# Kernel optimization log

Measured on AMD Instinct MI355X. Metric: run time of the kernel, lower is better.

Reference implementation:

```python
import jax, jax.numpy as jnp
import numpy as np

N, E = 50000, 1600000
C_IN, C_H, C_OUT = 36, 64, 64
EPS = 1e-16  # PyG softmax denominator epsilon


def setup_inputs() -> dict:
    key = jax.random.key(0)
    ks = jax.random.split(key, 48)
    inp = {}
    inp["features"] = jax.random.normal(ks[0], (N, C_IN), dtype=jnp.float32)
    inp["edge_attr"] = jax.random.uniform(ks[1], (E, 1), dtype=jnp.float32)
    inp["edge_index"] = jax.random.randint(ks[2], (2, E), 0, N, dtype=jnp.int32)
    dims = [(C_IN, C_H), (C_H, C_H), (C_H, C_H), (C_H, C_OUT)]
    i = 3
    for l, (din, dout) in enumerate(dims, 1):
        s = 1.0 / np.sqrt(din)
        inp[f"Wl{l}"] = jax.random.normal(ks[i], (din, dout), jnp.float32) * s; i += 1
        inp[f"bl{l}"] = jax.random.normal(ks[i], (dout,), jnp.float32) * 0.02; i += 1
        inp[f"Wr{l}"] = jax.random.normal(ks[i], (din, dout), jnp.float32) * s; i += 1
        inp[f"br{l}"] = jax.random.normal(ks[i], (dout,), jnp.float32) * 0.02; i += 1
        inp[f"We{l}"] = jax.random.normal(ks[i], (1, dout), jnp.float32); i += 1
        inp[f"att{l}"] = jax.random.normal(ks[i], (dout,), jnp.float32) * s; i += 1
        inp[f"bo{l}"] = jax.random.normal(ks[i], (dout,), jnp.float32) * 0.02; i += 1
    mlp = [(C_OUT, C_OUT // 2, "m1"), (C_OUT // 2, C_OUT // 4, "m2"), (C_OUT // 4, 1, "m3")]
    for din, dout, tag in mlp:
        s = 1.0 / np.sqrt(din)
        inp[f"W{tag}"] = jax.random.normal(ks[i], (din, dout), jnp.float32) * s; i += 1
        inp[f"b{tag}"] = jax.random.normal(ks[i], (dout,), jnp.float32) * 0.02; i += 1
    return inp


def gatv2_conv(x, src, dst, edge_attr, Wl, bl, Wr, br, We, att, bo):
    """Single-head GATv2Conv with edge features (PyG semantics)."""
    xl = x @ Wl + bl                      # [N, dout] source transform
    xr = x @ Wr + br                      # [N, dout] target transform
    ea = edge_attr @ We                   # [E, dout]
    e = jax.nn.leaky_relu(xl[src] + xr[dst] + ea, 0.2)  # [E, dout]
    score = e @ att                       # [E]
    # segment softmax over edges sharing a destination node
    m = jax.ops.segment_max(score, dst, num_segments=N)
    a = jnp.exp(score - m[dst])
    denom = jax.ops.segment_sum(a, dst, num_segments=N)
    alpha = a / (denom[dst] + EPS)
    out = jax.ops.segment_sum(xl[src] * alpha[:, None], dst, num_segments=N)
    return out + bo


def reference(features, edge_attr, edge_index,
              Wl1, bl1, Wr1, br1, We1, att1, bo1,
              Wl2, bl2, Wr2, br2, We2, att2, bo2,
              Wl3, bl3, Wr3, br3, We3, att3, bo3,
              Wl4, bl4, Wr4, br4, We4, att4, bo4,
              Wm1, bm1, Wm2, bm2, Wm3, bm3):
    src, dst = edge_index[0], edge_index[1]
    x = jax.nn.relu(gatv2_conv(features, src, dst, edge_attr, Wl1, bl1, Wr1, br1, We1, att1, bo1))
    x = jax.nn.relu(gatv2_conv(x, src, dst, edge_attr, Wl2, bl2, Wr2, br2, We2, att2, bo2))
    x = jax.nn.relu(gatv2_conv(x, src, dst, edge_attr, Wl3, bl3, Wr3, br3, We3, att3, bo3))
    x = jax.nn.relu(gatv2_conv(x, src, dst, edge_attr, Wl4, bl4, Wr4, br4, We4, att4, bo4))
    x = jnp.mean(x, axis=-2)              # graph readout -> [C_OUT]
    x = jax.nn.relu(x @ Wm1 + bm1)
    x = jax.nn.relu(x @ Wm2 + bm2)
    return x @ Wm3 + bm3                  # [1]
```

## Files before the change

kernel.cpp:

```cpp
#include <hip/hip_runtime.h>


__device__ __forceinline__ int rfl(int v) { return __builtin_amdgcn_readfirstlane(v); }

#define NBK_MAX 256

__global__ void __launch_bounds__(256) k_bcount(const int* __restrict__ dst,
                                                int* __restrict__ bkcnt, int E, int nbk) {
  __shared__ int cnt[NBK_MAX];
  int tid = threadIdx.x;
  if (tid < nbk) cnt[tid] = 0;
  __syncthreads();
  int base = blockIdx.x * 4096 + tid;
  #pragma unroll
  for (int k = 0; k < 16; k++) {
    int e = base + k * 256;
    if (e < E) atomicAdd(&cnt[((unsigned)dst[e]) >> 8], 1);
  }
  __syncthreads();
  if (tid < nbk) {
    int c = cnt[tid];
    if (c > 0) atomicAdd(&bkcnt[tid * 16], c);
  }
}

__global__ void k_bscan(const int* __restrict__ bkcnt, int* __restrict__ boffs,
                        int nbk, int E) {
  __shared__ int wsum[4];
  int tid = threadIdx.x, lane = tid & 63, wv = tid >> 6;
  int v = (tid < nbk) ? bkcnt[tid * 16] : 0;
  int x = v;
  #pragma unroll
  for (int o = 1; o < 64; o <<= 1) {
    int t = __shfl_up(x, o, 64);
    if (lane >= o) x += t;
  }
  if (lane == 63) wsum[wv] = x;
  __syncthreads();
  int wo = 0;
  for (int k = 0; k < 4; k++) if (k < wv) wo += wsum[k];
  if (tid < nbk) boffs[tid] = wo + (x - v);
  if (tid == 0) boffs[nbk] = E;
}

__global__ void __launch_bounds__(256) k_scatter(
    const int* __restrict__ src, const int* __restrict__ dst,
    const float* __restrict__ ea_in, const int* __restrict__ boffs,
    int* __restrict__ bcur, uint2* __restrict__ tmp, int E, int nbk) {
  __shared__ int cnt[NBK_MAX];
  __shared__ int cur[NBK_MAX];
  __shared__ int gbase[NBK_MAX];
  __shared__ int sbase[NBK_MAX];
  int tid = threadIdx.x;
  if (tid < nbk) {
    cnt[tid] = 0;
    cur[tid] = 0;
    sbase[tid] = boffs[tid];
  }
  __syncthreads();
  int base = blockIdx.x * 4096 + tid;
  uint2 rec[16];
  #pragma unroll
  for (int k = 0; k < 16; k++) {
    int e = base + k * 256;
    if (e < E) {
      unsigned d = (unsigned)dst[e];
      rec[k] = make_uint2((d << 16) | (unsigned)src[e],
                          (unsigned)__float_as_int(ea_in[e]));
      atomicAdd(&cnt[d >> 8], 1);
    } else {
      rec[k] = make_uint2(0u, 0u);
    }
  }
  __syncthreads();
  if (tid < nbk) {
    int c = cnt[tid];
    gbase[tid] = (c > 0) ? atomicAdd(&bcur[tid * 16], c) : 0;
  }
  __syncthreads();
  #pragma unroll
  for (int k = 0; k < 16; k++) {
    int e = base + k * 256;
    if (e < E) {
      int b = (int)(rec[k].x >> 24);
      int slot = atomicAdd(&cur[b], 1);
      tmp[sbase[b] + gbase[b] + slot] = rec[k];
    }
  }
}

__global__ void __launch_bounds__(256) k_csr(const int* __restrict__ boffs,
                                             const uint2* __restrict__ tmp,
                                             int2* __restrict__ pairs,
                                             int* __restrict__ rowptr, int N) {
  __shared__ int cnt[256];
  __shared__ int pref[256];
  __shared__ int cur[256];
  __shared__ int wsum[4];
  int b = blockIdx.x;
  int n0 = b << 8;
  int tid = threadIdx.x, lane = tid & 63, wv = tid >> 6;
  cnt[tid] = 0;
  cur[tid] = 0;
  __syncthreads();
  int lo = boffs[b], hi = boffs[b + 1];
  for (int k = lo + tid; k < hi; k += 256)
    atomicAdd(&cnt[(int)(tmp[k].x >> 16) - n0], 1);
  __syncthreads();
  int v = cnt[tid];
  int x = v;
  #pragma unroll
  for (int o = 1; o < 64; o <<= 1) {
    int t = __shfl_up(x, o, 64);
    if (lane >= o) x += t;
  }
  if (lane == 63) wsum[wv] = x;
  __syncthreads();
  int wo = 0;
  for (int k = 0; k < 4; k++) if (k < wv) wo += wsum[k];
  int start = lo + wo + (x - v);
  pref[tid] = start;
  int nn = n0 + tid;
  if (nn <= N) rowptr[nn] = start;
  __syncthreads();
  for (int k = lo + tid; k < hi; k += 256) {
    uint2 rec = tmp[k];
    int local = (int)(rec.x >> 16) - n0;
    int pos = pref[local] + atomicAdd(&cur[local], 1);
    pairs[pos] = make_int2((int)(rec.x & 0xffffu), (int)rec.y);
  }
}

template <int DIN, int TILES>
__global__ void __launch_bounds__(256) k_transform(
    const float* __restrict__ x, const float* __restrict__ Wl, const float* __restrict__ bl,
    const float* __restrict__ Wr, const float* __restrict__ br,
    float* __restrict__ xl, float* __restrict__ xr, int nNodes) {
  __shared__ __align__(16) float sWl[DIN * 64];
  __shared__ __align__(16) float sWr[DIN * 64];
  __shared__ float sx[16][DIN + 1];
  int tid = threadIdx.x;
  for (int i = tid; i < DIN * 64; i += 256) { sWl[i] = Wl[i]; sWr[i] = Wr[i]; }
  int node = tid >> 4;
  int t4 = (tid & 15) * 4;
  float4 bl4 = *(const float4*)(bl + t4);
  float4 br4 = *(const float4*)(br + t4);
  for (int t = 0; t < TILES; t++) {
    int nb = (blockIdx.x * TILES + t) * 16;
    if (nb >= nNodes) break;
    __syncthreads();
    for (int i = tid; i < 16 * DIN; i += 256) {
      int ln = i / DIN, c = i % DIN;
      int g = nb + ln;
      sx[ln][c] = (g < nNodes) ? x[(size_t)g * DIN + c] : 0.f;
    }
    __syncthreads();
    float4 accl = bl4;
    float4 accr = br4;
    const float* xrow = sx[node];
    #pragma unroll 4
    for (int k = 0; k < DIN; k++) {
      float xv = xrow[k];
      float4 wl = *(const float4*)(sWl + k * 64 + t4);
      float4 wr = *(const float4*)(sWr + k * 64 + t4);
      accl.x = fmaf(xv, wl.x, accl.x); accl.y = fmaf(xv, wl.y, accl.y);
      accl.z = fmaf(xv, wl.z, accl.z); accl.w = fmaf(xv, wl.w, accl.w);
      accr.x = fmaf(xv, wr.x, accr.x); accr.y = fmaf(xv, wr.y, accr.y);
      accr.z = fmaf(xv, wr.z, accr.z); accr.w = fmaf(xv, wr.w, accr.w);
    }
    int g = nb + node;
    if (g < nNodes) {
      *(float4*)(xl + (size_t)g * 64 + t4) = accl;
      *(float4*)(xr + (size_t)g * 64 + t4) = accr;
    }
  }
}

#define SC1(T, EA, OUT) { float u, acc; \
  u = T.x + fmaf(EA, We4.x, xr4.x); u = fmaxf(u, 0.2f * u); acc = at4.x * u; \
  u = T.y + fmaf(EA, We4.y, xr4.y); u = fmaxf(u, 0.2f * u); acc = fmaf(at4.y, u, acc); \
  u = T.z + fmaf(EA, We4.z, xr4.z); u = fmaxf(u, 0.2f * u); acc = fmaf(at4.z, u, acc); \
  u = T.w + fmaf(EA, We4.w, xr4.w); u = fmaxf(u, 0.2f * u); acc = fmaf(at4.w, u, acc); \
  OUT = acc; }

__global__ void __launch_bounds__(256, 5) k_edge(
    const float* __restrict__ xl, const float* __restrict__ xr,
    const int* __restrict__ rowptr, const int2* __restrict__ pairs,
    const float* __restrict__ We, const float* __restrict__ att,
    const float* __restrict__ bo, float* __restrict__ xout, int nNodes) {
  int lane = threadIdx.x & 63;
  int wv = rfl((int)(threadIdx.x >> 6));
  int n = rfl(blockIdx.x * 4 + wv);
  if (n >= nNodes) return;
  int c4 = lane & 15;
  int r  = lane >> 4;
  int cb = c4 * 4;

  float4 We4 = *(const float4*)(We + cb);
  float4 at4 = *(const float4*)(att + cb);
  float4 xr4 = *(const float4*)(xr + (size_t)n * 64 + cb);
  int s0 = rfl(rowptr[n]);
  int s1 = rfl(rowptr[n + 1]);
  int last = s1 - 1;

  float m = -3.0e38f, d = 0.f;
  float4 A = {0.f, 0.f, 0.f, 0.f};

  for (int kb = s0; kb < s1; kb += 16) {
    int cnt = rfl(min(16, s1 - kb));
    int2 p0 = pairs[min(kb + r,      last)];
    int2 p1 = pairs[min(kb + 4 + r,  last)];
    int2 p2 = pairs[min(kb + 8 + r,  last)];
    int2 p3 = pairs[min(kb + 12 + r, last)];
    float ea0 = __int_as_float(p0.y);
    float ea1 = __int_as_float(p1.y);
    float ea2 = __int_as_float(p2.y);
    float ea3 = __int_as_float(p3.y);

    float4 t0 = *(const float4*)(xl + (size_t)(unsigned)p0.x * 64 + cb);
    float4 t1 = *(const float4*)(xl + (size_t)(unsigned)p1.x * 64 + cb);
    float4 t2 = *(const float4*)(xl + (size_t)(unsigned)p2.x * 64 + cb);
    float4 t3 = *(const float4*)(xl + (size_t)(unsigned)p3.x * 64 + cb);

    float sc0, sc1, sc2, sc3;
    SC1(t0, ea0, sc0)
    SC1(t1, ea1, sc1)
    SC1(t2, ea2, sc2)
    SC1(t3, ea3, sc3)

    #pragma unroll
    for (int o = 1; o <= 8; o <<= 1) {
      sc0 += __shfl_xor(sc0, o, 64);
      sc1 += __shfl_xor(sc1, o, 64);
      sc2 += __shfl_xor(sc2, o, 64);
      sc3 += __shfl_xor(sc3, o, 64);
    }
    sc0 = (r < cnt)      ? sc0 : -3.0e38f;
    sc1 = (4 + r < cnt)  ? sc1 : -3.0e38f;
    sc2 = (8 + r < cnt)  ? sc2 : -3.0e38f;
    sc3 = (12 + r < cnt) ? sc3 : -3.0e38f;

    float mc = fmaxf(fmaxf(sc0, sc1), fmaxf(sc2, sc3));
    mc = fmaxf(mc, __shfl_xor(mc, 16, 64));
    mc = fmaxf(mc, __shfl_xor(mc, 32, 64));
    float newm = fmaxf(m, mc);
    float rf = __expf(m - newm);
    float a0 = __expf(sc0 - newm);
    float a1 = __expf(sc1 - newm);
    float a2 = __expf(sc2 - newm);
    float a3 = __expf(sc3 - newm);
    float ds = (a0 + a1) + (a2 + a3);
    ds += __shfl_xor(ds, 16, 64);
    ds += __shfl_xor(ds, 32, 64);
    d = d * rf + ds;
    m = newm;

    A.x = fmaf(a0, t0.x, A.x * rf); A.y = fmaf(a0, t0.y, A.y * rf);
    A.z = fmaf(a0, t0.z, A.z * rf); A.w = fmaf(a0, t0.w, A.w * rf);
    A.x = fmaf(a1, t1.x, A.x); A.y = fmaf(a1, t1.y, A.y);
    A.z = fmaf(a1, t1.z, A.z); A.w = fmaf(a1, t1.w, A.w);
    A.x = fmaf(a2, t2.x, A.x); A.y = fmaf(a2, t2.y, A.y);
    A.z = fmaf(a2, t2.z, A.z); A.w = fmaf(a2, t2.w, A.w);
    A.x = fmaf(a3, t3.x, A.x); A.y = fmaf(a3, t3.y, A.y);
    A.z = fmaf(a3, t3.z, A.z); A.w = fmaf(a3, t3.w, A.w);
  }

  A.x += __shfl_xor(A.x, 16, 64); A.y += __shfl_xor(A.y, 16, 64);
  A.z += __shfl_xor(A.z, 16, 64); A.w += __shfl_xor(A.w, 16, 64);
  A.x += __shfl_xor(A.x, 32, 64); A.y += __shfl_xor(A.y, 32, 64);
  A.z += __shfl_xor(A.z, 32, 64); A.w += __shfl_xor(A.w, 32, 64);

  float inv = 1.f / (d + 1e-16f);
  if (r == 0) {
    float4 bo4 = *(const float4*)(bo + cb);
    float4 o4;
    o4.x = fmaxf(fmaf(A.x, inv, bo4.x), 0.f);
    o4.y = fmaxf(fmaf(A.y, inv, bo4.y), 0.f);
    o4.z = fmaxf(fmaf(A.z, inv, bo4.z), 0.f);
    o4.w = fmaxf(fmaf(A.w, inv, bo4.w), 0.f);
    *(float4*)(xout + (size_t)n * 64 + cb) = o4;
  }
}

__global__ void k_mean(const float* __restrict__ x, double* __restrict__ meanbuf, int nNodes) {
  __shared__ float sacc[256];
  int lane = threadIdx.x & 63;
  int wv = threadIdx.x >> 6;
  int gw = blockIdx.x * 4 + wv;
  int stride = gridDim.x * 4;
  float acc = 0.f;
  for (int n = gw; n < nNodes; n += stride) acc += x[(size_t)n * 64 + lane];
  sacc[threadIdx.x] = acc;
  __syncthreads();
  if (threadIdx.x < 64) {
    float a = sacc[threadIdx.x] + sacc[threadIdx.x + 64] + sacc[threadIdx.x + 128] + sacc[threadIdx.x + 192];
    atomicAdd(&meanbuf[lane], (double)a);
  }
}

__global__ void k_mlp(const double* __restrict__ meanbuf,
                      const float* __restrict__ Wm1, const float* __restrict__ bm1,
                      const float* __restrict__ Wm2, const float* __restrict__ bm2,
                      const float* __restrict__ Wm3, const float* __restrict__ bm3,
                      float* __restrict__ out, double invN) {
  __shared__ float xm[64];
  __shared__ float h1[32];
  __shared__ float h2[16];
  int t = threadIdx.x;
  xm[t] = (float)(meanbuf[t] * invN);
  __syncthreads();
  if (t < 32) {
    float a = bm1[t];
    for (int c = 0; c < 64; c++) a = fmaf(xm[c], Wm1[c * 32 + t], a);
    h1[t] = fmaxf(a, 0.f);
  }
  __syncthreads();
  if (t < 16) {
    float a = bm2[t];
    for (int c = 0; c < 32; c++) a = fmaf(h1[c], Wm2[c * 16 + t], a);
    h2[t] = fmaxf(a, 0.f);
  }
  __syncthreads();
  if (t == 0) {
    float a = bm3[0];
    for (int c = 0; c < 16; c++) a = fmaf(h2[c], Wm3[c], a);
    out[0] = a;
  }
}

extern "C" void kernel_launch(void* const* d_in, const int* in_sizes, int n_in,
                              void* d_out, int out_size, void* d_ws, size_t ws_size,
                              hipStream_t stream) {
  (void)n_in; (void)out_size; (void)ws_size;
  const int N = in_sizes[0] / 36;
  const int E = in_sizes[1];

  const float* feat = (const float*)d_in[0];
  const float* eat  = (const float*)d_in[1];
  const int*   eidx = (const int*)d_in[2];
  const int* src = eidx;
  const int* dst = eidx + E;

  const float* L[4][7];
  for (int l = 0; l < 4; l++)
    for (int j = 0; j < 7; j++) L[l][j] = (const float*)d_in[3 + l * 7 + j];
  const float* Wm1 = (const float*)d_in[31];
  const float* bm1 = (const float*)d_in[32];
  const float* Wm2 = (const float*)d_in[33];
  const float* bm2 = (const float*)d_in[34];
  const float* Wm3 = (const float*)d_in[35];
  const float* bm3 = (const float*)d_in[36];

  const int NBK = (N + 255) >> 8;

  char* ws = (char*)d_ws;
  size_t off = 0;
  auto alloc = [&](size_t bytes) {
    off = (off + 511) & ~(size_t)511;
    void* p = ws + off;
    off += bytes;
    return p;
  };
  int*    bkcnt   = (int*)alloc((size_t)NBK * 16 * 4);
  int*    bcur    = (int*)alloc((size_t)NBK * 16 * 4);
  double* meanbuf = (double*)alloc(64 * 8);
  size_t zero_bytes = off;
  int*    boffs   = (int*)alloc((size_t)(NBK + 1) * 4);
  int*    rowptr  = (int*)alloc((size_t)(N + 1) * 4);
  int2*   pairs   = (int2*)alloc((size_t)E * 8);
  float*  xA      = (float*)alloc((size_t)N * 64 * 4);
  float*  xB      = (float*)alloc((size_t)N * 64 * 4);
  float*  xC      = (float*)alloc((size_t)N * 64 * 4);
  uint2*  tmp     = (uint2*)xC;

  hipMemsetAsync(d_ws, 0, zero_bytes, stream);

  const int TILES = 4;
  int sgrid = (E + 4095) / 4096;
  int tgrid = (N + 16 * TILES - 1) / (16 * TILES);
  int ngrid = (N + 3) / 4;

  k_bcount<<<sgrid, 256, 0, stream>>>(dst, bkcnt, E, NBK);
  k_bscan<<<1, 256, 0, stream>>>(bkcnt, boffs, NBK, E);
  k_scatter<<<sgrid, 256, 0, stream>>>(src, dst, eat, boffs, bcur, tmp, E, NBK);
  k_csr<<<NBK, 256, 0, stream>>>(boffs, tmp, pairs, rowptr, N);

  for (int l = 0; l < 4; l++) {
    if (l == 0)
      k_transform<36, TILES><<<tgrid, 256, 0, stream>>>(feat, L[0][0], L[0][1], L[0][2], L[0][3], xA, xB, N);
    else
      k_transform<64, TILES><<<tgrid, 256, 0, stream>>>(xC, L[l][0], L[l][1], L[l][2], L[l][3], xA, xB, N);
    k_edge<<<ngrid, 256, 0, stream>>>(xA, xB, rowptr, pairs,
                                      L[l][4], L[l][5], L[l][6], xC, N);
  }

  k_mean<<<256, 256, 0, stream>>>(xC, meanbuf, N);
  k_mlp<<<1, 64, 0, stream>>>(meanbuf, Wm1, bm1, Wm2, bm2, Wm3, bm3, (float*)d_out, 1.0 / (double)N);
}
```

Baseline: 519.5 us.

## Drop bucket count pass with fixed-capacity buckets; register-tile node transform

```diff
diff --git a/kernel.cpp b/kernel.cpp
--- a/kernel.cpp
+++ b/kernel.cpp
@@ -4,59 +4,17 @@
 __device__ __forceinline__ int rfl(int v) { return __builtin_amdgcn_readfirstlane(v); }
 
 #define NBK_MAX 256
-
-__global__ void __launch_bounds__(256) k_bcount(const int* __restrict__ dst,
-                                                int* __restrict__ bkcnt, int E, int nbk) {
-  __shared__ int cnt[NBK_MAX];
-  int tid = threadIdx.x;
-  if (tid < nbk) cnt[tid] = 0;
-  __syncthreads();
-  int base = blockIdx.x * 4096 + tid;
-  #pragma unroll
-  for (int k = 0; k < 16; k++) {
-    int e = base + k * 256;
-    if (e < E) atomicAdd(&cnt[((unsigned)dst[e]) >> 8], 1);
-  }
-  __syncthreads();
-  if (tid < nbk) {
-    int c = cnt[tid];
-    if (c > 0) atomicAdd(&bkcnt[tid * 16], c);
-  }
-}
-
-__global__ void k_bscan(const int* __restrict__ bkcnt, int* __restrict__ boffs,
-                        int nbk, int E) {
-  __shared__ int wsum[4];
-  int tid = threadIdx.x, lane = tid & 63, wv = tid >> 6;
-  int v = (tid < nbk) ? bkcnt[tid * 16] : 0;
-  int x = v;
-  #pragma unroll
-  for (int o = 1; o < 64; o <<= 1) {
-    int t = __shfl_up(x, o, 64);
-    if (lane >= o) x += t;
-  }
-  if (lane == 63) wsum[wv] = x;
-  __syncthreads();
-  int wo = 0;
-  for (int k = 0; k < 4; k++) if (k < wv) wo += wsum[k];
-  if (tid < nbk) boffs[tid] = wo + (x - v);
-  if (tid == 0) boffs[nbk] = E;
-}
+#define BCAP 10240
 
 __global__ void __launch_bounds__(256) k_scatter(
     const int* __restrict__ src, const int* __restrict__ dst,
-    const float* __restrict__ ea_in, const int* __restrict__ boffs,
+    const float* __restrict__ ea_in,
     int* __restrict__ bcur, uint2* __restrict__ tmp, int E, int nbk) {
   __shared__ int cnt[NBK_MAX];
   __shared__ int cur[NBK_MAX];
   __shared__ int gbase[NBK_MAX];
-  __shared__ int sbase[NBK_MAX];
   int tid = threadIdx.x;
-  if (tid < nbk) {
-    cnt[tid] = 0;
-    cur[tid] = 0;
-    sbase[tid] = boffs[tid];
-  }
+  if (tid < nbk) { cnt[tid] = 0; cur[tid] = 0; }
   __syncthreads();
   int base = blockIdx.x * 4096 + tid;
   uint2 rec[16];
@@ -84,12 +42,32 @@
     if (e < E) {
       int b = (int)(rec[k].x >> 24);
       int slot = atomicAdd(&cur[b], 1);
-      tmp[sbase[b] + gbase[b] + slot] = rec[k];
+      tmp[(size_t)b * BCAP + gbase[b] + slot] = rec[k];
     }
   }
 }
 
-__global__ void __launch_bounds__(256) k_csr(const int* __restrict__ boffs,
+__global__ void k_bscan(const int* __restrict__ bcur, int* __restrict__ boffs,
+                        int nbk, int E) {
+  __shared__ int wsum[4];
+  int tid = threadIdx.x, lane = tid & 63, wv = tid >> 6;
+  int v = (tid < nbk) ? bcur[tid * 16] : 0;
+  int x = v;
+  #pragma unroll
+  for (int o = 1; o < 64; o <<= 1) {
+    int t = __shfl_up(x, o, 64);
+    if (lane >= o) x += t;
+  }
+  if (lane == 63) wsum[wv] = x;
+  __syncthreads();
+  int wo = 0;
+  for (int k = 0; k < 4; k++) if (k < wv) wo += wsum[k];
+  if (tid < nbk) boffs[tid] = wo + (x - v);
+  if (tid == 0) boffs[nbk] = E;
+}
+
+__global__ void __launch_bounds__(256) k_csr(const int* __restrict__ bcur,
+                                             const int* __restrict__ boffs,
                                              const uint2* __restrict__ tmp,
                                              int2* __restrict__ pairs,
                                              int* __restrict__ rowptr, int N) {
@@ -103,9 +81,11 @@
   cnt[tid] = 0;
   cur[tid] = 0;
   __syncthreads();
-  int lo = boffs[b], hi = boffs[b + 1];
-  for (int k = lo + tid; k < hi; k += 256)
-    atomicAdd(&cnt[(int)(tmp[k].x >> 16) - n0], 1);
+  int cb = bcur[b * 16];
+  const uint2* tb = tmp + (size_t)b * BCAP;
+  int lo = boffs[b];
+  for (int k = tid; k < cb; k += 256)
+    atomicAdd(&cnt[(int)(tb[k].x >> 16) - n0], 1);
   __syncthreads();
   int v = cnt[tid];
   int x = v;
@@ -123,57 +103,68 @@
   int nn = n0 + tid;
   if (nn <= N) rowptr[nn] = start;
   __syncthreads();
-  for (int k = lo + tid; k < hi; k += 256) {
-    uint2 rec = tmp[k];
+  for (int k = tid; k < cb; k += 256) {
+    uint2 rec = tb[k];
     int local = (int)(rec.x >> 16) - n0;
     int pos = pref[local] + atomicAdd(&cur[local], 1);
     pairs[pos] = make_int2((int)(rec.x & 0xffffu), (int)rec.y);
   }
 }
 
-template <int DIN, int TILES>
+template <int DIN>
 __global__ void __launch_bounds__(256) k_transform(
     const float* __restrict__ x, const float* __restrict__ Wl, const float* __restrict__ bl,
     const float* __restrict__ Wr, const float* __restrict__ br,
     float* __restrict__ xl, float* __restrict__ xr, int nNodes) {
   __shared__ __align__(16) float sWl[DIN * 64];
   __shared__ __align__(16) float sWr[DIN * 64];
-  __shared__ float sx[16][DIN + 1];
+  __shared__ float sx[64][DIN + 1];
   int tid = threadIdx.x;
   for (int i = tid; i < DIN * 64; i += 256) { sWl[i] = Wl[i]; sWr[i] = Wr[i]; }
-  int node = tid >> 4;
-  int t4 = (tid & 15) * 4;
-  float4 bl4 = *(const float4*)(bl + t4);
-  float4 br4 = *(const float4*)(br + t4);
-  for (int t = 0; t < TILES; t++) {
-    int nb = (blockIdx.x * TILES + t) * 16;
-    if (nb >= nNodes) break;
-    __syncthreads();
-    for (int i = tid; i < 16 * DIN; i += 256) {
-      int ln = i / DIN, c = i % DIN;
-      int g = nb + ln;
-      sx[ln][c] = (g < nNodes) ? x[(size_t)g * DIN + c] : 0.f;
-    }
-    __syncthreads();
-    float4 accl = bl4;
-    float4 accr = br4;
-    const float* xrow = sx[node];
-    #pragma unroll 4
-    for (int k = 0; k < DIN; k++) {
-      float xv = xrow[k];
-      float4 wl = *(const float4*)(sWl + k * 64 + t4);
-      float4 wr = *(const float4*)(sWr + k * 64 + t4);
-      accl.x = fmaf(xv, wl.x, accl.x); accl.y = fmaf(xv, wl.y, accl.y);
-      accl.z = fmaf(xv, wl.z, accl.z); accl.w = fmaf(xv, wl.w, accl.w);
-      accr.x = fmaf(xv, wr.x, accr.x); accr.y = fmaf(xv, wr.y, accr.y);
-      accr.z = fmaf(xv, wr.z, accr.z); accr.w = fmaf(xv, wr.w, accr.w);
-    }
-    int g = nb + node;
-    if (g < nNodes) {
-      *(float4*)(xl + (size_t)g * 64 + t4) = accl;
-      *(float4*)(xr + (size_t)g * 64 + t4) = accr;
-    }
-  }
+  int nb = blockIdx.x * 64;
+  for (int i = tid; i < 64 * DIN; i += 256) {
+    int ln = i / DIN, c = i % DIN;
+    int g = nb + ln;
+    sx[ln][c] = (g < nNodes) ? x[(size_t)g * DIN + c] : 0.f;
+  }
+  __syncthreads();
+  int c4 = (tid & 15) * 4;
+  int ns = (tid >> 4) * 4;
+  float4 bl4 = *(const float4*)(bl + c4);
+  float4 br4 = *(const float4*)(br + c4);
+  float4 L0 = bl4, L1 = bl4, L2 = bl4, L3 = bl4;
+  float4 R0 = br4, R1 = br4, R2 = br4, R3 = br4;
+  const float* x0 = sx[ns + 0];
+  const float* x1 = sx[ns + 1];
+  const float* x2 = sx[ns + 2];
+  const float* x3 = sx[ns + 3];
+  #pragma unroll 4
+  for (int k = 0; k < DIN; k++) {
+    float4 wl = *(const float4*)(sWl + k * 64 + c4);
+    float4 wr = *(const float4*)(sWr + k * 64 + c4);
+    float a = x0[k], bb = x1[k], c = x2[k], dd = x3[k];
+    L0.x = fmaf(a, wl.x, L0.x);  L0.y = fmaf(a, wl.y, L0.y);
+    L0.z = fmaf(a, wl.z, L0.z);  L0.w = fmaf(a, wl.w, L0.w);
+    R0.x = fmaf(a, wr.x, R0.x);  R0.y = fmaf(a, wr.y, R0.y);
+    R0.z = fmaf(a, wr.z, R0.z);  R0.w = fmaf(a, wr.w, R0.w);
+    L1.x = fmaf(bb, wl.x, L1.x); L1.y = fmaf(bb, wl.y, L1.y);
+    L1.z = fmaf(bb, wl.z, L1.z); L1.w = fmaf(bb, wl.w, L1.w);
+    R1.x = fmaf(bb, wr.x, R1.x); R1.y = fmaf(bb, wr.y, R1.y);
+    R1.z = fmaf(bb, wr.z, R1.z); R1.w = fmaf(bb, wr.w, R1.w);
+    L2.x = fmaf(c, wl.x, L2.x);  L2.y = fmaf(c, wl.y, L2.y);
+    L2.z = fmaf(c, wl.z, L2.z);  L2.w = fmaf(c, wl.w, L2.w);
+    R2.x = fmaf(c, wr.x, R2.x);  R2.y = fmaf(c, wr.y, R2.y);
+    R2.z = fmaf(c, wr.z, R2.z);  R2.w = fmaf(c, wr.w, R2.w);
+    L3.x = fmaf(dd, wl.x, L3.x); L3.y = fmaf(dd, wl.y, L3.y);
+    L3.z = fmaf(dd, wl.z, L3.z); L3.w = fmaf(dd, wl.w, L3.w);
+    R3.x = fmaf(dd, wr.x, R3.x); R3.y = fmaf(dd, wr.y, R3.y);
+    R3.z = fmaf(dd, wr.z, R3.z); R3.w = fmaf(dd, wr.w, R3.w);
+  }
+  int g = nb + ns;
+  if (g + 0 < nNodes) { *(float4*)(xl + (size_t)(g+0)*64 + c4) = L0; *(float4*)(xr + (size_t)(g+0)*64 + c4) = R0; }
+  if (g + 1 < nNodes) { *(float4*)(xl + (size_t)(g+1)*64 + c4) = L1; *(float4*)(xr + (size_t)(g+1)*64 + c4) = R1; }
+  if (g + 2 < nNodes) { *(float4*)(xl + (size_t)(g+2)*64 + c4) = L2; *(float4*)(xr + (size_t)(g+2)*64 + c4) = R2; }
+  if (g + 3 < nNodes) { *(float4*)(xl + (size_t)(g+3)*64 + c4) = L3; *(float4*)(xr + (size_t)(g+3)*64 + c4) = R3; }
 }
 
 #define SC1(T, EA, OUT) { float u, acc; \
@@ -361,7 +352,6 @@
     off += bytes;
     return p;
   };
-  int*    bkcnt   = (int*)alloc((size_t)NBK * 16 * 4);
   int*    bcur    = (int*)alloc((size_t)NBK * 16 * 4);
   double* meanbuf = (double*)alloc(64 * 8);
   size_t zero_bytes = off;
@@ -371,25 +361,23 @@
   float*  xA      = (float*)alloc((size_t)N * 64 * 4);
   float*  xB      = (float*)alloc((size_t)N * 64 * 4);
   float*  xC      = (float*)alloc((size_t)N * 64 * 4);
-  uint2*  tmp     = (uint2*)xC;
+  uint2*  tmp     = (uint2*)xB;
 
   hipMemsetAsync(d_ws, 0, zero_bytes, stream);
 
-  const int TILES = 4;
   int sgrid = (E + 4095) / 4096;
-  int tgrid = (N + 16 * TILES - 1) / (16 * TILES);
+  int tgrid = (N + 63) / 64;
   int ngrid = (N + 3) / 4;
 
-  k_bcount<<<sgrid, 256, 0, stream>>>(dst, bkcnt, E, NBK);
-  k_bscan<<<1, 256, 0, stream>>>(bkcnt, boffs, NBK, E);
-  k_scatter<<<sgrid, 256, 0, stream>>>(src, dst, eat, boffs, bcur, tmp, E, NBK);
-  k_csr<<<NBK, 256, 0, stream>>>(boffs, tmp, pairs, rowptr, N);
+  k_scatter<<<sgrid, 256, 0, stream>>>(src, dst, eat, bcur, tmp, E, NBK);
+  k_bscan<<<1, 256, 0, stream>>>(bcur, boffs, NBK, E);
+  k_csr<<<NBK, 256, 0, stream>>>(bcur, boffs, tmp, pairs, rowptr, N);
 
   for (int l = 0; l < 4; l++) {
     if (l == 0)
-      k_transform<36, TILES><<<tgrid, 256, 0, stream>>>(feat, L[0][0], L[0][1], L[0][2], L[0][3], xA, xB, N);
+      k_transform<36><<<tgrid, 256, 0, stream>>>(feat, L[0][0], L[0][1], L[0][2], L[0][3], xA, xB, N);
     else
-      k_transform<64, TILES><<<tgrid, 256, 0, stream>>>(xC, L[l][0], L[l][1], L[l][2], L[l][3], xA, xB, N);
+      k_transform<64><<<tgrid, 256, 0, stream>>>(xC, L[l][0], L[l][1], L[l][2], L[l][3], xA, xB, N);
     k_edge<<<ngrid, 256, 0, stream>>>(xA, xB, rowptr, pairs,
                                       L[l][4], L[l][5], L[l][6], xC, N);
   }
```

Result: faster. 497.6 us (-4.2%).
